# Kernel tuning notes

Measured on AMD Instinct MI355X. Metric: run time of the kernel, lower is better.

Reference implementation:

```python
import jax, jax.numpy as jnp
import numpy as np

NEG = -1e9

def setup_inputs() -> dict:
    key = jax.random.key(0)
    ks = jax.random.split(key, 8)
    B, Lc, Lq, D = 64, 1024, 128, 128
    C = jax.random.normal(ks[0], (B, Lc, D), dtype=jnp.float32)
    Q = jax.random.normal(ks[1], (B, Lq, D), dtype=jnp.float32)
    Cmask = jax.random.randint(ks[2], (B, Lc), 0, 2, dtype=jnp.int32)
    Qmask = jax.random.randint(ks[3], (B, Lq), 0, 2, dtype=jnp.int32)
    w_c = jax.random.normal(ks[4], (D, 1), dtype=jnp.float32) * (6.0 / (D + 1)) ** 0.5
    w_q = jax.random.normal(ks[5], (D, 1), dtype=jnp.float32) * (6.0 / (D + 1)) ** 0.5
    w_mul = jax.random.normal(ks[6], (1, 1, D), dtype=jnp.float32) * (6.0 / (D + 1)) ** 0.5
    bias = jnp.zeros((1,), dtype=jnp.float32)
    return {"C": C, "Q": Q, "Cmask": Cmask, "Qmask": Qmask,
            "w_c": w_c, "w_q": w_q, "w_mul": w_mul, "bias": bias}

def reference(C, Q, Cmask, Qmask, w_c, w_q, w_mul, bias):
    # Optimized trilinear similarity: S[b,i,j] = C.w_c + Q.w_q + (C*w_mul).Q^T + bias
    s0 = jnp.matmul(C, w_c)                        # [B,Lc,1]
    s1 = jnp.swapaxes(jnp.matmul(Q, w_q), 1, 2)    # [B,1,Lq]
    s2 = jnp.einsum('bid,bjd->bij', C * w_mul, Q)  # [B,Lc,Lq]
    S = s0 + s1 + s2 + bias
    qmask = (Qmask[:, None, :] == 0)               # [B,1,Lq]
    cmask = (Cmask[:, :, None] == 0)               # [B,Lc,1]
    S1 = jax.nn.softmax(jnp.where(qmask, NEG, S), axis=2)
    S2 = jax.nn.softmax(jnp.where(cmask, NEG, S), axis=1)
    A = jnp.matmul(S1, Q)                                       # [B,Lc,D]
    Bm = jnp.matmul(jnp.matmul(S1, jnp.swapaxes(S2, 1, 2)), C)  # [B,Lc,D]
    return jnp.concatenate([C, A, C * A, C * Bm], axis=2)
```

## Files before the change

kernel.cpp:

```cpp
#include <hip/hip_runtime.h>
#include <math.h>

constexpr int Bn = 64, Lc = 1024, Lq = 128, Dd = 128;

typedef __attribute__((ext_vector_type(8))) short short8_t;
typedef __attribute__((ext_vector_type(4))) short short4_t;
typedef __attribute__((ext_vector_type(4))) float f32x4;

__device__ __forceinline__ short f2bf(float x) {
    unsigned u = __float_as_uint(x);
    u += 0x7FFFu + ((u >> 16) & 1u);
    return (short)(u >> 16);
}

constexpr int AS = 132;
constexpr int TS = 70;
constexpr int CTS = 68;
constexpr int PS = 68;
constexpr int TBS = 36;

__device__ __forceinline__ void decode_bid(int n, int& b, int& blk) {
    b = (n & 7) * 8 + ((n >> 3) & 7);
    blk = n >> 6;
}

__global__ __launch_bounds__(256) void k1_fused(
    const float* __restrict__ C, const float* __restrict__ Q,
    const int* __restrict__ Cmask, const int* __restrict__ Qmask,
    const float* __restrict__ w_c, const float* __restrict__ w_q,
    const float* __restrict__ w_mul, const float* __restrict__ bias,
    short* __restrict__ CW16, short* __restrict__ CT16,
    short* __restrict__ Q16, short* __restrict__ QT16,
    float* __restrict__ s0f, float* __restrict__ s1f,
    float* __restrict__ colpart, float* __restrict__ rowsumInv)
{
    __shared__ short Abuf[64 * AS];
    __shared__ short Bbuf[128 * AS];
    __shared__ float s0L[64], cmL[64], s1L[128], qmL[128];
    __shared__ float colL[4 * 128];
    short* Tbuf = Bbuf;

    int b, blk; decode_bid(blockIdx.x, b, blk);
    int i0 = blk * 64, tid = threadIdx.x;

    const float4* C4 = (const float4*)(C + ((size_t)(b * Lc + i0)) * Dd);
    #pragma unroll
    for (int k = 0; k < 8; ++k) {
        int idx = tid + k * 256;
        int i = idx >> 5, d4 = idx & 31;
        float4 v = C4[idx];
        float4 wm = ((const float4*)w_mul)[d4];
        short4_t cw; cw[0]=f2bf(v.x*wm.x); cw[1]=f2bf(v.y*wm.y); cw[2]=f2bf(v.z*wm.z); cw[3]=f2bf(v.w*wm.w);
        *(short4_t*)&Abuf[i * AS + d4 * 4] = cw;
        float cm = (Cmask[b * Lc + i0 + i] != 0) ? 1.0f : 0.0f;
        Tbuf[(d4*4+0)*TS + i] = f2bf(cm * v.x);
        Tbuf[(d4*4+1)*TS + i] = f2bf(cm * v.y);
        Tbuf[(d4*4+2)*TS + i] = f2bf(cm * v.z);
        Tbuf[(d4*4+3)*TS + i] = f2bf(cm * v.w);
        float4 wc = ((const float4*)w_c)[d4];
        float dot = v.x*wc.x + v.y*wc.y + v.z*wc.z + v.w*wc.w;
        #pragma unroll
        for (int off = 1; off < 32; off <<= 1) dot += __shfl_xor(dot, off, 64);
        if ((tid & 31) == 0) { s0L[i] = dot; cmL[i] = cm; s0f[b * Lc + i0 + i] = dot; }
    }
    __syncthreads();

    #pragma unroll
    for (int k = 0; k < 8; ++k) {
        int idx = tid + k * 256;
        int d = idx >> 4, i4 = idx & 15;
        *(short4_t*)&CT16[((size_t)(b * Dd + d)) * Lc + i0 + i4 * 4] =
            *(short4_t*)&Tbuf[d * TS + i4 * 4];
    }
    #pragma unroll
    for (int k = 0; k < 4; ++k) {
        int idx = tid + k * 256;
        int i = idx >> 4, h = idx & 15;
        *(short8_t*)&CW16[((size_t)(b * Lc + i0 + i)) * Dd + h * 8] =
            *(short8_t*)&Abuf[i * AS + h * 8];
    }
    __syncthreads();

    const float4* Q4 = (const float4*)(Q + (size_t)b * Lq * Dd);
    #pragma unroll
    for (int k = 0; k < 16; ++k) {
        int idx = tid + k * 256;
        int j = idx >> 5, d4 = idx & 31;
        float4 v = Q4[idx];
        short4_t qv; qv[0]=f2bf(v.x); qv[1]=f2bf(v.y); qv[2]=f2bf(v.z); qv[3]=f2bf(v.w);
        *(short4_t*)&Bbuf[j * AS + d4 * 4] = qv;
        float4 wq = ((const float4*)w_q)[d4];
        float dot = v.x*wq.x + v.y*wq.y + v.z*wq.z + v.w*wq.w;
        #pragma unroll
        for (int off = 1; off < 32; off <<= 1) dot += __shfl_xor(dot, off, 64);
        if ((tid & 31) == 0) {
            s1L[j] = dot;
            qmL[j] = (Qmask[b * Lq + j] != 0) ? 1.0f : 0.0f;
            if (blk == 0) s1f[b * Lq + j] = dot;
        }
    }
    __syncthreads();

    int w = tid >> 6, lane = tid & 63, lm = lane & 15, quad = lane >> 4;
    int iw = i0 + w * 16;
    f32x4 acc[8];
    #pragma unroll
    for (int t = 0; t < 8; ++t) acc[t] = (f32x4){0.f,0.f,0.f,0.f};
    #pragma unroll
    for (int ks = 0; ks < 4; ++ks) {
        short8_t a = *(short8_t*)&Abuf[(w * 16 + lm) * AS + ks * 32 + quad * 8];
        #pragma unroll
        for (int jt = 0; jt < 8; ++jt) {
            short8_t bf = *(short8_t*)&Bbuf[(jt * 16 + lm) * AS + ks * 32 + quad * 8];
            acc[jt] = __builtin_amdgcn_mfma_f32_16x16x32_bf16(a, bf, acc[jt], 0, 0, 0);
        }
    }

    float s0v[4], cmv[4];
    #pragma unroll
    for (int r = 0; r < 4; ++r) {
        s0v[r] = s0L[w * 16 + quad * 4 + r];
        cmv[r] = cmL[w * 16 + quad * 4 + r];
    }
    float bb = bias[0];
    float rowpart[4] = {0.f, 0.f, 0.f, 0.f};
    #pragma unroll
    for (int jt = 0; jt < 8; ++jt) {
        int j = jt * 16 + lm;
        float s1 = s1L[j] + bb;
        float qm = qmL[j];
        float cs = 0.f;
        #pragma unroll
        for (int r = 0; r < 4; ++r) {
            float e = __expf(acc[jt][r] + s0v[r] + s1);
            rowpart[r] += qm * e;
            cs += cmv[r] * e;
        }
        cs += __shfl_xor(cs, 16, 64);
        cs += __shfl_xor(cs, 32, 64);
        if (lane < 16) colL[w * 128 + j] = cs;
    }
    #pragma unroll
    for (int r = 0; r < 4; ++r) {
        float v = rowpart[r];
        v += __shfl_xor(v, 1, 64); v += __shfl_xor(v, 2, 64);
        v += __shfl_xor(v, 4, 64); v += __shfl_xor(v, 8, 64);
        if (lm == 0) rowsumInv[b * Lc + iw + quad * 4 + r] = 1.0f / v;
    }
    __syncthreads();
    if (tid < 128)
        colpart[((size_t)b * 16 + blk) * Lq + tid] =
            colL[tid] + colL[128 + tid] + colL[256 + tid] + colL[384 + tid];

    if (blk == 0) {
        #pragma unroll
        for (int k = 0; k < 8; ++k) {
            int idx = tid + k * 256;
            int j = idx >> 4, h = idx & 15;
            *(short8_t*)&Q16[((size_t)(b * Lq + j)) * Dd + h * 8] =
                *(short8_t*)&Bbuf[j * AS + h * 8];
        }
        #pragma unroll
        for (int k = 0; k < 16; ++k) {
            int idx = tid + k * 256;
            int d = idx >> 5, j4 = idx & 31;
            short4_t o;
            #pragma unroll
            for (int r = 0; r < 4; ++r) {
                int j = j4 * 4 + r;
                o[r] = (qmL[j] != 0.f) ? Bbuf[j * AS + d] : (short)0;
            }
            *(short4_t*)&QT16[((size_t)(b * Dd + d)) * Lq + j4 * 4] = o;
        }
    }
}

__global__ __launch_bounds__(512) void k2_T(
    const short* __restrict__ CW16, const short* __restrict__ CT16,
    const short* __restrict__ Q16, const float* __restrict__ s0f,
    const float* __restrict__ s1f, const float* __restrict__ bias,
    const int* __restrict__ Qmask, const float* __restrict__ colpart,
    short* __restrict__ TT16)
{
    __shared__ short Qs[32 * AS];
    __shared__ short CWs[64 * AS];
    __shared__ short CTs[128 * CTS];
    __shared__ short Ps[32 * PS];
    __shared__ float s1bL[32], invqL[32], s0L[64];

    int n = blockIdx.x;
    int b, jq; decode_bid(n, b, jq);
    int tid = threadIdx.x, w = tid >> 6, lane = tid & 63;
    int lm = lane & 15, quad = lane >> 4;
    int jh = w & 1, ih = w >> 1;

    {
        int j = tid >> 4, h = tid & 15;
        *(short8_t*)&Qs[j * AS + h * 8] =
            *(const short8_t*)&Q16[((size_t)(b * Lq + jq * 32 + j)) * Dd + h * 8];
    }
    if (tid < 32) {
        int j = jq * 32 + tid;
        s1bL[tid] = s1f[b * Lq + j] + bias[0];
        float cs = 0.f;
        #pragma unroll
        for (int p = 0; p < 16; ++p) cs += colpart[((size_t)b * 16 + p) * Lq + j];
        invqL[tid] = (Qmask[b * Lq + j] != 0) ? 1.0f / cs : 0.0f;
    }

    const short* CWb = CW16 + (size_t)b * Lc * Dd;
    const short* CTb = CT16 + (size_t)b * Dd * Lc;
    int iA0 = tid >> 4, iA1 = 32 + (tid >> 4), hA0 = (tid & 15) * 8;
    int dB0 = tid >> 3, dB1 = 64 + (tid >> 3), hB0 = (tid & 7) * 8;

    short8_t wA0 = *(const short8_t*)&CWb[(size_t)iA0 * Dd + hA0];
    short8_t wA1 = *(const short8_t*)&CWb[(size_t)iA1 * Dd + hA0];
    short8_t wB0 = *(const short8_t*)&CTb[(size_t)dB0 * Lc + hB0];
    short8_t wB1 = *(const short8_t*)&CTb[(size_t)dB1 * Lc + hB0];
    float s0r = (tid < 64) ? s0f[b * Lc + tid] : 0.f;

    f32x4 acc2[2];
    acc2[0] = (f32x4){0.f,0.f,0.f,0.f};
    acc2[1] = (f32x4){0.f,0.f,0.f,0.f};

    for (int ic = 0; ic < 16; ++ic) {
        __syncthreads();
        *(short8_t*)&CWs[iA0 * AS + hA0] = wA0;
        *(short8_t*)&CWs[iA1 * AS + hA0] = wA1;
        *(short8_t*)&CTs[dB0 * CTS + hB0] = wB0;
        *(short8_t*)&CTs[dB1 * CTS + hB0] = wB1;
        if (tid < 64) s0L[tid] = s0r;
        if (ic < 15) {
            int ibn = (ic + 1) * 64;
            wA0 = *(const short8_t*)&CWb[((size_t)(ibn + iA0)) * Dd + hA0];
            wA1 = *(const short8_t*)&CWb[((size_t)(ibn + iA1)) * Dd + hA0];
            wB0 = *(const short8_t*)&CTb[(size_t)dB0 * Lc + ibn + hB0];
            wB1 = *(const short8_t*)&CTb[(size_t)dB1 * Lc + ibn + hB0];
            if (tid < 64) s0r = s0f[b * Lc + ibn + tid];
        }
        __syncthreads();

        f32x4 sacc = (f32x4){0.f,0.f,0.f,0.f};
        #pragma unroll
        for (int ks = 0; ks < 4; ++ks) {
            short8_t a = *(short8_t*)&Qs[(jh * 16 + lm) * AS + ks * 32 + quad * 8];
            short8_t bf = *(short8_t*)&CWs[(ih * 16 + lm) * AS + ks * 32 + quad * 8];
            sacc = __builtin_amdgcn_mfma_f32_16x16x32_bf16(a, bf, sacc, 0, 0, 0);
        }
        float s0v = s0L[ih * 16 + lm];
        #pragma unroll
        for (int r = 0; r < 4; ++r) {
            float e = __expf(sacc[r] + s0v + s1bL[jh * 16 + quad * 4 + r]);
            Ps[(jh * 16 + quad * 4 + r) * PS + ih * 16 + lm] = f2bf(e);
        }
        __syncthreads();

        #pragma unroll
        for (int ks = 0; ks < 2; ++ks) {
            short8_t a = *(short8_t*)&Ps[(jh * 16 + lm) * PS + ks * 32 + quad * 8];
            #pragma unroll
            for (int t = 0; t < 2; ++t) {
                short8_t bf = *(short8_t*)&CTs[((ih * 2 + t) * 16 + lm) * CTS + ks * 32 + quad * 8];
                acc2[t] = __builtin_amdgcn_mfma_f32_16x16x32_bf16(a, bf, acc2[t], 0, 0, 0);
            }
        }
    }

    short* Tb = CWs;
    #pragma unroll
    for (int t = 0; t < 2; ++t) {
        int d = (ih * 2 + t) * 16 + lm;
        #pragma unroll
        for (int r = 0; r < 4; ++r) {
            int jl = jh * 16 + quad * 4 + r;
            Tb[d * TBS + jl] = f2bf(acc2[t][r] * invqL[jl]);
        }
    }
    __syncthreads();
    #pragma unroll
    for (int k = 0; k < 2; ++k) {
        int idx = tid + k * 512;
        int d = idx >> 3, j4 = idx & 7;
        *(short4_t*)&TT16[((size_t)(b * Dd + d)) * Lq + jq * 32 + j4 * 4] =
            *(short4_t*)&Tb[d * TBS + j4 * 4];
    }
}

__global__ __launch_bounds__(256) void k3_out(
    const short* __restrict__ Q16, const short* __restrict__ QT16,
    const short* __restrict__ TT16, const float* __restrict__ C,
    const float* __restrict__ w_mul, const float* __restrict__ s0f,
    const float* __restrict__ s1f, const float* __restrict__ bias,
    const float* __restrict__ rowsumInv, float* __restrict__ out)
{
    __shared__ short Abuf[64 * AS];
    __shared__ short Bbuf[128 * AS];
    __shared__ float s0L[64], s1bL[128];
    float* Af32 = (float*)Bbuf;

    int n = blockIdx.x;
    int b, blk; decode_bid(n, b, blk);
    int i0 = blk * 64, tid = threadIdx.x;
    int w = tid >> 6, lane = tid & 63, lm = lane & 15, quad = lane >> 4;
    int iw = i0 + w * 16;

    const short8_t* Qg = (const short8_t*)(Q16 + (size_t)b * Lq * Dd);
    #pragma unroll
    for (int k = 0; k < 8; ++k) {
        int idx = tid + k * 256;
        int j = idx >> 4, h = idx & 15;
        *(short8_t*)&Bbuf[j * AS + h * 8] = Qg[idx];
    }
    const float4* C4 = (const float4*)(C + ((size_t)(b * Lc + i0)) * Dd);
    float4 cv[8];
    #pragma unroll
    for (int k = 0; k < 8; ++k) {
        int idx = tid + k * 256;
        int i = idx >> 5, d4 = idx & 31;
        float4 v = C4[idx];
        cv[k] = v;
        float4 wm = ((const float4*)w_mul)[d4];
        short4_t cw; cw[0]=f2bf(v.x*wm.x); cw[1]=f2bf(v.y*wm.y); cw[2]=f2bf(v.z*wm.z); cw[3]=f2bf(v.w*wm.w);
        *(short4_t*)&Abuf[i * AS + d4 * 4] = cw;
    }
    if (tid < 64) s0L[tid] = s0f[b * Lc + i0 + tid];
    if (tid >= 128 && tid < 256) s1bL[tid - 128] = s1f[b * Lq + tid - 128] + bias[0];
    __syncthreads();

    f32x4 acc[8];
    #pragma unroll
    for (int t = 0; t < 8; ++t) acc[t] = (f32x4){0.f,0.f,0.f,0.f};
    #pragma unroll
    for (int ks = 0; ks < 4; ++ks) {
        short8_t a = *(short8_t*)&Abuf[(w * 16 + lm) * AS + ks * 32 + quad * 8];
        #pragma unroll
        for (int jt = 0; jt < 8; ++jt) {
            short8_t bf = *(short8_t*)&Bbuf[(jt * 16 + lm) * AS + ks * 32 + quad * 8];
            acc[jt] = __builtin_amdgcn_mfma_f32_16x16x32_bf16(a, bf, acc[jt], 0, 0, 0);
        }
    }
    float s0v[4];
    #pragma unroll
    for (int r = 0; r < 4; ++r) s0v[r] = s0L[w * 16 + quad * 4 + r];
    #pragma unroll
    for (int jt = 0; jt < 8; ++jt) {
        int j = jt * 16 + lm;
        float s1b = s1bL[j];
        #pragma unroll
        for (int r = 0; r < 4; ++r) {
            float e = __expf(acc[jt][r] + s0v[r] + s1b);
            Abuf[(w * 16 + quad * 4 + r) * AS + j] = f2bf(e);
        }
    }
    __syncthreads();

    const short8_t* QTg = (const short8_t*)(QT16 + (size_t)b * Dd * Lq);
    #pragma unroll
    for (int k = 0; k < 8; ++k) {
        int idx = tid + k * 256;
        int d = idx >> 4, h = idx & 15;
        *(short8_t*)&Bbuf[d * AS + h * 8] = QTg[idx];
    }
    float rs[4];
    #pragma unroll
    for (int r = 0; r < 4; ++r) rs[r] = rowsumInv[b * Lc + iw + quad * 4 + r];
    __syncthreads();
    f32x4 accQ[8];
    #pragma unroll
    for (int t = 0; t < 8; ++t) accQ[t] = (f32x4){0.f,0.f,0.f,0.f};
    #pragma unroll
    for (int ks = 0; ks < 4; ++ks) {
        short8_t a = *(short8_t*)&Abuf[(w * 16 + lm) * AS + ks * 32 + quad * 8];
        #pragma unroll
        for (int dt = 0; dt < 8; ++dt) {
            short8_t bf = *(short8_t*)&Bbuf[(dt * 16 + lm) * AS + ks * 32 + quad * 8];
            accQ[dt] = __builtin_amdgcn_mfma_f32_16x16x32_bf16(a, bf, accQ[dt], 0, 0, 0);
        }
    }
    __syncthreads();

    const short8_t* TTg = (const short8_t*)(TT16 + (size_t)b * Dd * Lq);
    #pragma unroll
    for (int k = 0; k < 8; ++k) {
        int idx = tid + k * 256;
        int d = idx >> 4, h = idx & 15;
        *(short8_t*)&Bbuf[d * AS + h * 8] = TTg[idx];
    }
    __syncthreads();
    f32x4 accT[8];
    #pragma unroll
    for (int t = 0; t < 8; ++t) accT[t] = (f32x4){0.f,0.f,0.f,0.f};
    #pragma unroll
    for (int ks = 0; ks < 4; ++ks) {
        short8_t a = *(short8_t*)&Abuf[(w * 16 + lm) * AS + ks * 32 + quad * 8];
        #pragma unroll
        for (int dt = 0; dt < 8; ++dt) {
            short8_t bf = *(short8_t*)&Bbuf[(dt * 16 + lm) * AS + ks * 32 + quad * 8];
            accT[dt] = __builtin_amdgcn_mfma_f32_16x16x32_bf16(a, bf, accT[dt], 0, 0, 0);
        }
    }
    __syncthreads();

    #pragma unroll
    for (int dt = 0; dt < 8; ++dt)
        #pragma unroll
        for (int r = 0; r < 4; ++r)
            Af32[(w * 16 + quad * 4 + r) * AS + dt * 16 + lm] = accQ[dt][r] * rs[r];
    __syncthreads();

    #pragma unroll
    for (int k = 0; k < 8; ++k) {
        int idx = tid + k * 256;
        int i = idx >> 5, d4 = idx & 31;
        float4 av = *(float4*)&Af32[i * AS + d4 * 4];
        float4 c = cv[k];
        size_t base = ((size_t)(b * Lc + i0 + i)) * (4 * Dd) + d4 * 4;
        *(float4*)&out[base]           = c;
        *(float4*)&out[base + Dd]      = av;
        float4 ca; ca.x = c.x*av.x; ca.y = c.y*av.y; ca.z = c.z*av.z; ca.w = c.w*av.w;
        *(float4*)&out[base + 2 * Dd]  = ca;
    }
    __syncthreads();

    #pragma unroll
    for (int dt = 0; dt < 8; ++dt)
        #pragma unroll
        for (int r = 0; r < 4; ++r)
            Af32[(w * 16 + quad * 4 + r) * AS + dt * 16 + lm] = accT[dt][r] * rs[r];
    __syncthreads();

    #pragma unroll
    for (int k = 0; k < 8; ++k) {
        int idx = tid + k * 256;
        int i = idx >> 5, d4 = idx & 31;
        float4 bm = *(float4*)&Af32[i * AS + d4 * 4];
        float4 c = cv[k];
        size_t base = ((size_t)(b * Lc + i0 + i)) * (4 * Dd) + d4 * 4;
        float4 cb; cb.x = c.x*bm.x; cb.y = c.y*bm.y; cb.z = c.z*bm.z; cb.w = c.w*bm.w;
        *(float4*)&out[base + 3 * Dd]  = cb;
    }
}

extern "C" void kernel_launch(void* const* d_in, const int* in_sizes, int n_in,
                              void* d_out, int out_size, void* d_ws, size_t ws_size,
                              hipStream_t stream) {
    const float* C     = (const float*)d_in[0];
    const float* Q     = (const float*)d_in[1];
    const int*   Cmask = (const int*)d_in[2];
    const int*   Qmask = (const int*)d_in[3];
    const float* w_c   = (const float*)d_in[4];
    const float* w_q   = (const float*)d_in[5];
    const float* w_mul = (const float*)d_in[6];
    const float* bias  = (const float*)d_in[7];
    float* out = (float*)d_out;

    char* p = (char*)d_ws;
    const size_t ND = (size_t)Bn * Lc * Dd;
    const size_t NQ = (size_t)Bn * Lq * Dd;
    short* CW16 = (short*)p; p += ND * 2;
    short* CT16 = (short*)p; p += ND * 2;
    short* Q16  = (short*)p; p += NQ * 2;
    short* QT16 = (short*)p; p += NQ * 2;
    short* TT16 = (short*)p; p += NQ * 2;
    float* s0f       = (float*)p; p += (size_t)Bn * Lc * 4;
    float* s1f       = (float*)p; p += (size_t)Bn * Lq * 4;
    float* colpart   = (float*)p; p += (size_t)Bn * 16 * Lq * 4;
    float* rowsumInv = (float*)p; p += (size_t)Bn * Lc * 4;

    k1_fused<<<dim3(1024), 256, 0, stream>>>(C, Q, Cmask, Qmask, w_c, w_q, w_mul, bias,
                                             CW16, CT16, Q16, QT16, s0f, s1f, colpart, rowsumInv);
    k2_T<<<dim3(256), 512, 0, stream>>>(CW16, CT16, Q16, s0f, s1f, bias, Qmask, colpart, TT16);
    k3_out<<<dim3(1024), 256, 0, stream>>>(Q16, QT16, TT16, C, w_mul, s0f, s1f, bias, rowsumInv, out);
}
```

Before: 249.0 us.

## Drop CW16 intermediate, recompute C*w_mul in k2, trim LDS and registers

```diff
diff --git a/kernel.cpp b/kernel.cpp
--- a/kernel.cpp
+++ b/kernel.cpp
@@ -24,12 +24,12 @@
     blk = n >> 6;
 }
 
-__global__ __launch_bounds__(256) void k1_fused(
+__global__ __launch_bounds__(256, 3) void k1_fused(
     const float* __restrict__ C, const float* __restrict__ Q,
     const int* __restrict__ Cmask, const int* __restrict__ Qmask,
     const float* __restrict__ w_c, const float* __restrict__ w_q,
     const float* __restrict__ w_mul, const float* __restrict__ bias,
-    short* __restrict__ CW16, short* __restrict__ CT16,
+    short* __restrict__ CT16,
     short* __restrict__ Q16, short* __restrict__ QT16,
     float* __restrict__ s0f, float* __restrict__ s1f,
     float* __restrict__ colpart, float* __restrict__ rowsumInv)
@@ -37,7 +37,6 @@
     __shared__ short Abuf[64 * AS];
     __shared__ short Bbuf[128 * AS];
     __shared__ float s0L[64], cmL[64], s1L[128], qmL[128];
-    __shared__ float colL[4 * 128];
     short* Tbuf = Bbuf;
 
     int b, blk; decode_bid(blockIdx.x, b, blk);
@@ -72,13 +71,6 @@
         *(short4_t*)&CT16[((size_t)(b * Dd + d)) * Lc + i0 + i4 * 4] =
             *(short4_t*)&Tbuf[d * TS + i4 * 4];
     }
-    #pragma unroll
-    for (int k = 0; k < 4; ++k) {
-        int idx = tid + k * 256;
-        int i = idx >> 4, h = idx & 15;
-        *(short8_t*)&CW16[((size_t)(b * Lc + i0 + i)) * Dd + h * 8] =
-            *(short8_t*)&Abuf[i * AS + h * 8];
-    }
     __syncthreads();
 
     const float4* Q4 = (const float4*)(Q + (size_t)b * Lq * Dd);
@@ -115,42 +107,6 @@
             acc[jt] = __builtin_amdgcn_mfma_f32_16x16x32_bf16(a, bf, acc[jt], 0, 0, 0);
         }
     }
-
-    float s0v[4], cmv[4];
-    #pragma unroll
-    for (int r = 0; r < 4; ++r) {
-        s0v[r] = s0L[w * 16 + quad * 4 + r];
-        cmv[r] = cmL[w * 16 + quad * 4 + r];
-    }
-    float bb = bias[0];
-    float rowpart[4] = {0.f, 0.f, 0.f, 0.f};
-    #pragma unroll
-    for (int jt = 0; jt < 8; ++jt) {
-        int j = jt * 16 + lm;
-        float s1 = s1L[j] + bb;
-        float qm = qmL[j];
-        float cs = 0.f;
-        #pragma unroll
-        for (int r = 0; r < 4; ++r) {
-            float e = __expf(acc[jt][r] + s0v[r] + s1);
-            rowpart[r] += qm * e;
-            cs += cmv[r] * e;
-        }
-        cs += __shfl_xor(cs, 16, 64);
-        cs += __shfl_xor(cs, 32, 64);
-        if (lane < 16) colL[w * 128 + j] = cs;
-    }
-    #pragma unroll
-    for (int r = 0; r < 4; ++r) {
-        float v = rowpart[r];
-        v += __shfl_xor(v, 1, 64); v += __shfl_xor(v, 2, 64);
-        v += __shfl_xor(v, 4, 64); v += __shfl_xor(v, 8, 64);
-        if (lm == 0) rowsumInv[b * Lc + iw + quad * 4 + r] = 1.0f / v;
-    }
-    __syncthreads();
-    if (tid < 128)
-        colpart[((size_t)b * 16 + blk) * Lq + tid] =
-            colL[tid] + colL[128 + tid] + colL[256 + tid] + colL[384 + tid];
 
     if (blk == 0) {
         #pragma unroll
@@ -173,12 +129,51 @@
             *(short4_t*)&QT16[((size_t)(b * Dd + d)) * Lq + j4 * 4] = o;
         }
     }
+    __syncthreads();
+
+    float* colL = (float*)Bbuf;
+    float s0v[4], cmv[4];
+    #pragma unroll
+    for (int r = 0; r < 4; ++r) {
+        s0v[r] = s0L[w * 16 + quad * 4 + r];
+        cmv[r] = cmL[w * 16 + quad * 4 + r];
+    }
+    float bb = bias[0];
+    float rowpart[4] = {0.f, 0.f, 0.f, 0.f};
+    #pragma unroll
+    for (int jt = 0; jt < 8; ++jt) {
+        int j = jt * 16 + lm;
+        float s1 = s1L[j] + bb;
+        float qm = qmL[j];
+        float cs = 0.f;
+        #pragma unroll
+        for (int r = 0; r < 4; ++r) {
+            float e = __expf(acc[jt][r] + s0v[r] + s1);
+            rowpart[r] += qm * e;
+            cs += cmv[r] * e;
+        }
+        cs += __shfl_xor(cs, 16, 64);
+        cs += __shfl_xor(cs, 32, 64);
+        if (lane < 16) colL[w * 128 + j] = cs;
+    }
+    #pragma unroll
+    for (int r = 0; r < 4; ++r) {
+        float v = rowpart[r];
+        v += __shfl_xor(v, 1, 64); v += __shfl_xor(v, 2, 64);
+        v += __shfl_xor(v, 4, 64); v += __shfl_xor(v, 8, 64);
+        if (lm == 0) rowsumInv[b * Lc + iw + quad * 4 + r] = 1.0f / v;
+    }
+    __syncthreads();
+    if (tid < 128)
+        colpart[((size_t)b * 16 + blk) * Lq + tid] =
+            colL[tid] + colL[128 + tid] + colL[256 + tid] + colL[384 + tid];
 }
 
 __global__ __launch_bounds__(512) void k2_T(
-    const short* __restrict__ CW16, const short* __restrict__ CT16,
+    const float* __restrict__ C, const short* __restrict__ CT16,
     const short* __restrict__ Q16, const float* __restrict__ s0f,
     const float* __restrict__ s1f, const float* __restrict__ bias,
+    const float* __restrict__ w_mul,
     const int* __restrict__ Qmask, const float* __restrict__ colpart,
     short* __restrict__ TT16)
 {
@@ -208,13 +203,16 @@
         invqL[tid] = (Qmask[b * Lq + j] != 0) ? 1.0f / cs : 0.0f;
     }
 
-    const short* CWb = CW16 + (size_t)b * Lc * Dd;
+    const float4* Cb4 = (const float4*)(C + (size_t)b * Lc * Dd);
     const short* CTb = CT16 + (size_t)b * Dd * Lc;
-    int iA0 = tid >> 4, iA1 = 32 + (tid >> 4), hA0 = (tid & 15) * 8;
+    int iS = tid >> 5, dS = tid & 31;
     int dB0 = tid >> 3, dB1 = 64 + (tid >> 3), hB0 = (tid & 7) * 8;
-
-    short8_t wA0 = *(const short8_t*)&CWb[(size_t)iA0 * Dd + hA0];
-    short8_t wA1 = *(const short8_t*)&CWb[(size_t)iA1 * Dd + hA0];
+    float4 wmv = ((const float4*)w_mul)[dS];
+
+    float4 pc[4];
+    #pragma unroll
+    for (int k = 0; k < 4; ++k)
+        pc[k] = Cb4[((size_t)(iS + k * 16)) * 32 + dS];
     short8_t wB0 = *(const short8_t*)&CTb[(size_t)dB0 * Lc + hB0];
     short8_t wB1 = *(const short8_t*)&CTb[(size_t)dB1 * Lc + hB0];
     float s0r = (tid < 64) ? s0f[b * Lc + tid] : 0.f;
@@ -225,15 +223,21 @@
 
     for (int ic = 0; ic < 16; ++ic) {
         __syncthreads();
-        *(short8_t*)&CWs[iA0 * AS + hA0] = wA0;
-        *(short8_t*)&CWs[iA1 * AS + hA0] = wA1;
+        #pragma unroll
+        for (int k = 0; k < 4; ++k) {
+            float4 v = pc[k];
+            short4_t cw;
+            cw[0]=f2bf(v.x*wmv.x); cw[1]=f2bf(v.y*wmv.y); cw[2]=f2bf(v.z*wmv.z); cw[3]=f2bf(v.w*wmv.w);
+            *(short4_t*)&CWs[(iS + k * 16) * AS + dS * 4] = cw;
+        }
         *(short8_t*)&CTs[dB0 * CTS + hB0] = wB0;
         *(short8_t*)&CTs[dB1 * CTS + hB0] = wB1;
         if (tid < 64) s0L[tid] = s0r;
         if (ic < 15) {
             int ibn = (ic + 1) * 64;
-            wA0 = *(const short8_t*)&CWb[((size_t)(ibn + iA0)) * Dd + hA0];
-            wA1 = *(const short8_t*)&CWb[((size_t)(ibn + iA1)) * Dd + hA0];
+            #pragma unroll
+            for (int k = 0; k < 4; ++k)
+                pc[k] = Cb4[((size_t)(ibn + iS + k * 16)) * 32 + dS];
             wB0 = *(const short8_t*)&CTb[(size_t)dB0 * Lc + ibn + hB0];
             wB1 = *(const short8_t*)&CTb[(size_t)dB1 * Lc + ibn + hB0];
             if (tid < 64) s0r = s0f[b * Lc + ibn + tid];
@@ -286,7 +290,7 @@
     }
 }
 
-__global__ __launch_bounds__(256) void k3_out(
+__global__ __launch_bounds__(256, 3) void k3_out(
     const short* __restrict__ Q16, const short* __restrict__ QT16,
     const short* __restrict__ TT16, const float* __restrict__ C,
     const float* __restrict__ w_mul, const float* __restrict__ s0f,
@@ -312,13 +316,11 @@
         *(short8_t*)&Bbuf[j * AS + h * 8] = Qg[idx];
     }
     const float4* C4 = (const float4*)(C + ((size_t)(b * Lc + i0)) * Dd);
-    float4 cv[8];
     #pragma unroll
     for (int k = 0; k < 8; ++k) {
         int idx = tid + k * 256;
         int i = idx >> 5, d4 = idx & 31;
         float4 v = C4[idx];
-        cv[k] = v;
         float4 wm = ((const float4*)w_mul)[d4];
         short4_t cw; cw[0]=f2bf(v.x*wm.x); cw[1]=f2bf(v.y*wm.y); cw[2]=f2bf(v.z*wm.z); cw[3]=f2bf(v.w*wm.w);
         *(short4_t*)&Abuf[i * AS + d4 * 4] = cw;
@@ -379,28 +381,6 @@
     }
     __syncthreads();
 
-    const short8_t* TTg = (const short8_t*)(TT16 + (size_t)b * Dd * Lq);
-    #pragma unroll
-    for (int k = 0; k < 8; ++k) {
-        int idx = tid + k * 256;
-        int d = idx >> 4, h = idx & 15;
-        *(short8_t*)&Bbuf[d * AS + h * 8] = TTg[idx];
-    }
-    __syncthreads();
-    f32x4 accT[8];
-    #pragma unroll
-    for (int t = 0; t < 8; ++t) accT[t] = (f32x4){0.f,0.f,0.f,0.f};
-    #pragma unroll
-    for (int ks = 0; ks < 4; ++ks) {
-        short8_t a = *(short8_t*)&Abuf[(w * 16 + lm) * AS + ks * 32 + quad * 8];
-        #pragma unroll
-        for (int dt = 0; dt < 8; ++dt) {
-            short8_t bf = *(short8_t*)&Bbuf[(dt * 16 + lm) * AS + ks * 32 + quad * 8];
-            accT[dt] = __builtin_amdgcn_mfma_f32_16x16x32_bf16(a, bf, accT[dt], 0, 0, 0);
-        }
-    }
-    __syncthreads();
-
     #pragma unroll
     for (int dt = 0; dt < 8; ++dt)
         #pragma unroll
@@ -413,7 +393,7 @@
         int idx = tid + k * 256;
         int i = idx >> 5, d4 = idx & 31;
         float4 av = *(float4*)&Af32[i * AS + d4 * 4];
-        float4 c = cv[k];
+        float4 c = C4[idx];
         size_t base = ((size_t)(b * Lc + i0 + i)) * (4 * Dd) + d4 * 4;
         *(float4*)&out[base]           = c;
         *(float4*)&out[base + Dd]      = av;
@@ -422,6 +402,28 @@
     }
     __syncthreads();
 
+    const short8_t* TTg = (const short8_t*)(TT16 + (size_t)b * Dd * Lq);
+    #pragma unroll
+    for (int k = 0; k < 8; ++k) {
+        int idx = tid + k * 256;
+        int d = idx >> 4, h = idx & 15;
+        *(short8_t*)&Bbuf[d * AS + h * 8] = TTg[idx];
+    }
+    __syncthreads();
+    f32x4 accT[8];
+    #pragma unroll
+    for (int t = 0; t < 8; ++t) accT[t] = (f32x4){0.f,0.f,0.f,0.f};
+    #pragma unroll
+    for (int ks = 0; ks < 4; ++ks) {
+        short8_t a = *(short8_t*)&Abuf[(w * 16 + lm) * AS + ks * 32 + quad * 8];
+        #pragma unroll
+        for (int dt = 0; dt < 8; ++dt) {
+            short8_t bf = *(short8_t*)&Bbuf[(dt * 16 + lm) * AS + ks * 32 + quad * 8];
+            accT[dt] = __builtin_amdgcn_mfma_f32_16x16x32_bf16(a, bf, accT[dt], 0, 0, 0);
+        }
+    }
+    __syncthreads();
+
     #pragma unroll
     for (int dt = 0; dt < 8; ++dt)
         #pragma unroll
@@ -434,7 +436,7 @@
         int idx = tid + k * 256;
         int i = idx >> 5, d4 = idx & 31;
         float4 bm = *(float4*)&Af32[i * AS + d4 * 4];
-        float4 c = cv[k];
+        float4 c = C4[idx];
         size_t base = ((size_t)(b * Lc + i0 + i)) * (4 * Dd) + d4 * 4;
         float4 cb; cb.x = c.x*bm.x; cb.y = c.y*bm.y; cb.z = c.z*bm.z; cb.w = c.w*bm.w;
         *(float4*)&out[base + 3 * Dd]  = cb;
@@ -457,7 +459,6 @@
     char* p = (char*)d_ws;
     const size_t ND = (size_t)Bn * Lc * Dd;
     const size_t NQ = (size_t)Bn * Lq * Dd;
-    short* CW16 = (short*)p; p += ND * 2;
     short* CT16 = (short*)p; p += ND * 2;
     short* Q16  = (short*)p; p += NQ * 2;
     short* QT16 = (short*)p; p += NQ * 2;
@@ -468,7 +469,7 @@
     float* rowsumInv = (float*)p; p += (size_t)Bn * Lc * 4;
 
     k1_fused<<<dim3(1024), 256, 0, stream>>>(C, Q, Cmask, Qmask, w_c, w_q, w_mul, bias,
-                                             CW16, CT16, Q16, QT16, s0f, s1f, colpart, rowsumInv);
-    k2_T<<<dim3(256), 512, 0, stream>>>(CW16, CT16, Q16, s0f, s1f, bias, Qmask, colpart, TT16);
+                                             CT16, Q16, QT16, s0f, s1f, colpart, rowsumInv);
+    k2_T<<<dim3(256), 512, 0, stream>>>(C, CT16, Q16, s0f, s1f, bias, w_mul, Qmask, colpart, TT16);
     k3_out<<<dim3(1024), 256, 0, stream>>>(Q16, QT16, TT16, C, w_mul, s0f, s1f, bias, rowsumInv, out);
 }
```

Measured after the change: 247.0 us. Within noise of the previous version (-0.8%).
